# Performance work log

Measured on AMD Instinct MI355X. Metric: run time of the kernel, lower is better.

Reference implementation:

```python
import jax, jax.numpy as jnp
import numpy as np

N_NODES = 50000
N_EDGES = 625000
FEAT = 128
NEG_SLOPE = 0.2  # dgl GATConv default leaky_relu slope


def setup_inputs() -> dict:
    key = jax.random.key(0)
    ks = jax.random.split(key, 16)
    x = jax.random.normal(ks[0], (N_NODES, FEAT), dtype=jnp.float32)
    src = jax.random.randint(ks[1], (N_EDGES,), 0, N_NODES, dtype=jnp.int32)
    dst = jax.random.randint(ks[2], (N_EDGES,), 0, N_NODES, dtype=jnp.int32)
    s = 1.0 / np.sqrt(FEAT)
    d = {"x": x, "src": src, "dst": dst}
    for i in range(3):
        d[f"W{i+1}"] = jax.random.normal(ks[3 + 4 * i], (FEAT, FEAT), dtype=jnp.float32) * s
        d[f"al{i+1}"] = jax.random.normal(ks[4 + 4 * i], (FEAT,), dtype=jnp.float32) * s
        d[f"ar{i+1}"] = jax.random.normal(ks[5 + 4 * i], (FEAT,), dtype=jnp.float32) * s
        d[f"b{i+1}"] = jnp.zeros((FEAT,), dtype=jnp.float32)
    return d


def gat_layer(h_in, src, dst, W, al, ar, b):
    # dgl GATConv, num_heads=1: fc -> edge attention -> edge_softmax -> scatter
    h = h_in @ W                                   # [N, F]
    el = h @ al                                    # [N]
    er = h @ ar                                    # [N]
    e = jax.nn.leaky_relu(el[src] + er[dst], NEG_SLOPE)   # [E]
    # numerically stable edge softmax, grouped by destination node
    m = jax.ops.segment_max(e, dst, num_segments=N_NODES)  # [N]
    ex = jnp.exp(e - m[dst])
    denom = jax.ops.segment_sum(ex, dst, num_segments=N_NODES)
    alpha = ex / denom[dst]                        # [E]
    out = jax.ops.segment_sum(alpha[:, None] * h[src], dst, num_segments=N_NODES)
    return out + b


def reference(x, src, dst, W1, al1, ar1, b1, W2, al2, ar2, b2, W3, al3, ar3, b3):
    h = gat_layer(x, src, dst, W1, al1, ar1, b1)
    h = jax.nn.relu(h)
    h = gat_layer(h, src, dst, W2, al2, ar2, b2)
    h = jax.nn.relu(h)
    h = gat_layer(h, src, dst, W3, al3, ar3, b3)
    return h
```

## Files before the change

kernel.cpp:

```cpp
#include <hip/hip_runtime.h>
#include <hip/hip_fp16.h>

#define N_NODES 50000
#define N_EDGES 625000
#define FEAT 128
#define NEG_SLOPE 0.2f
#define NB_SCAN 196

typedef __attribute__((ext_vector_type(8))) short bf16x8;
typedef __attribute__((ext_vector_type(4))) float f32x4;

__device__ __forceinline__ unsigned short f2bf(float f) {
  unsigned u = __float_as_uint(f);
  u += 0x7fffu + ((u >> 16) & 1u);
  return (unsigned short)(u >> 16);
}
__device__ __forceinline__ float bf2f(unsigned short s) {
  return __uint_as_float(((unsigned)s) << 16);
}


__global__ __launch_bounds__(256) void prepzero_kernel(
    const float* __restrict__ W0, const float* __restrict__ W1, const float* __restrict__ W2,
    unsigned short* __restrict__ wfhi, unsigned short* __restrict__ wflo,
    int* __restrict__ cnt) {
  int bb = blockIdx.x;
  if (bb < 192) {
    int idx = bb * 256 + threadIdx.x;
    if (idx >= 3 * FEAT * FEAT) return;
    int l = idx >> 14, rem = idx & 16383;
    int e = rem & 7, lane = (rem >> 3) & 63, kb = (rem >> 9) & 3, ct = rem >> 11;
    int col = ct * 16 + (lane & 15);
    int k   = kb * 32 + (lane >> 4) * 8 + e;
    const float* W = (l == 0) ? W0 : ((l == 1) ? W1 : W2);
    float v = W[k * FEAT + col];
    unsigned short hi = f2bf(v);
    wfhi[idx] = hi;
    wflo[idx] = f2bf(v - bf2f(hi));
  } else {
    int i = (bb - 192) * 256 + threadIdx.x;
    if (i < N_NODES + 16) cnt[i] = 0;
  }
}


__global__ __launch_bounds__(256) void hist_kernel(const int* __restrict__ dst,
                                                   int* __restrict__ cnt) {
  int e = blockIdx.x * 256 + threadIdx.x;
  if (e < N_EDGES) atomicAdd(&cnt[dst[e]], 1);
}

__global__ __launch_bounds__(256) void scan_part_kernel(const int* __restrict__ cnt,
                                                        int* __restrict__ part) {
  __shared__ int s[256];
  int i = blockIdx.x * 256 + threadIdx.x;
  s[threadIdx.x] = (i < N_NODES) ? cnt[i] : 0;
  __syncthreads();
  for (int o = 128; o > 0; o >>= 1) {
    if (threadIdx.x < o) s[threadIdx.x] += s[threadIdx.x + o];
    __syncthreads();
  }
  if (threadIdx.x == 0) part[blockIdx.x] = s[0];
}

__global__ __launch_bounds__(256) void scan_down_kernel(int* __restrict__ cnt,
                                                        const int* __restrict__ part,
                                                        int* __restrict__ offs) {
  __shared__ int s[256];
  __shared__ int sl[256];
  const int tid = threadIdx.x;

  int pv = (tid < NB_SCAN) ? part[tid] : 0;
  s[tid] = pv;
  __syncthreads();
  for (int o = 1; o < 256; o <<= 1) {
    int t = (tid >= o) ? s[tid - o] : 0;
    __syncthreads();
    s[tid] += t;
    __syncthreads();
  }
  const int blockPrefix = (blockIdx.x == 0) ? 0 : s[blockIdx.x - 1];
  if (blockIdx.x == 0 && tid == 0) offs[N_NODES] = s[NB_SCAN - 1];

  int i = blockIdx.x * 256 + tid;
  int v = (i < N_NODES) ? cnt[i] : 0;
  sl[tid] = v;
  __syncthreads();
  for (int o = 1; o < 256; o <<= 1) {
    int t = (tid >= o) ? sl[tid - o] : 0;
    __syncthreads();
    sl[tid] += t;
    __syncthreads();
  }
  if (i < N_NODES) {
    int excl = sl[tid] - v + blockPrefix;
    offs[i] = excl;
    cnt[i] = excl;
  }
}

__global__ __launch_bounds__(256) void fill_kernel(const int* __restrict__ src,
                                                   const int* __restrict__ dst,
                                                   int* __restrict__ cursor,
                                                   int* __restrict__ ssrc) {
  int e = blockIdx.x * 256 + threadIdx.x;
  if (e < N_EDGES) {
    int pos = atomicAdd(&cursor[dst[e]], 1);
    ssrc[pos] = src[e];
  }
}


__global__ __launch_bounds__(256) void gemm_mfma_kernel(
    const float* __restrict__ inF, const __half* __restrict__ inH,
    const unsigned short* __restrict__ wfhi, const unsigned short* __restrict__ wflo,
    const float* __restrict__ al, const float* __restrict__ ar,
    __half* __restrict__ h, float* __restrict__ el, float* __restrict__ er,
    int fp16relu_in)
{
  __shared__ __align__(16) char smem[32768];
  unsigned short* wl = (unsigned short*)smem;
  typedef __half (*tile_t)[132];
  tile_t tile = (tile_t)smem;

  const int tid = threadIdx.x;
  const int wave = tid >> 6, lane = tid & 63;
  const int lrow = lane & 15, lkb = lane >> 4;
  const int arow_i = blockIdx.x * 64 + wave * 16 + lrow;
  const bool avalid = arow_i < N_NODES;

#pragma unroll
  for (int q = 0; q < 8; ++q) {
    int idx = q * 256 + tid;
    int hilo = idx >> 10, r = idx & 1023, frag = r >> 6, word = r & 63;
    int ct = frag >> 1, kb = frag & 1;
    const uint4* s4 = (const uint4*)(hilo ? wflo : wfhi);
    uint4 v = s4[(ct * 4 + kb) * 64 + word];
    *(uint4*)&wl[((hilo * 16 + frag) << 9) + word * 8] = v;
  }

  bf16x8 ahi[4], alo[4];
#pragma unroll
  for (int kb = 0; kb < 4; ++kb) {
    float a[8];
    if (avalid) {
      if (fp16relu_in) {
        const unsigned short* aH = (const unsigned short*)inH + (size_t)arow_i * FEAT;
        uint4 rv = *(const uint4*)(aH + kb * 32 + lkb * 8);
        const __half2* hp = (const __half2*)&rv;
#pragma unroll
        for (int e2 = 0; e2 < 4; ++e2) {
          float2 f = __half22float2(hp[e2]);
          a[e2 * 2] = fmaxf(f.x, 0.f); a[e2 * 2 + 1] = fmaxf(f.y, 0.f);
        }
      } else {
        const float* arow = inF + (size_t)arow_i * FEAT;
        float4 v0 = *(const float4*)(arow + kb * 32 + lkb * 8);
        float4 v1 = *(const float4*)(arow + kb * 32 + lkb * 8 + 4);
        a[0] = v0.x; a[1] = v0.y; a[2] = v0.z; a[3] = v0.w;
        a[4] = v1.x; a[5] = v1.y; a[6] = v1.z; a[7] = v1.w;
      }
    } else {
#pragma unroll
      for (int e = 0; e < 8; ++e) a[e] = 0.f;
    }
#pragma unroll
    for (int e = 0; e < 8; ++e) {
      unsigned short hb = f2bf(a[e]);
      ahi[kb][e] = (short)hb;
      alo[kb][e] = (short)f2bf(a[e] - bf2f(hb));
    }
  }

  f32x4 acc[8];
#pragma unroll
  for (int ct = 0; ct < 8; ++ct)
#pragma unroll
    for (int r = 0; r < 4; ++r) acc[ct][r] = 0.f;

  __syncthreads();
#pragma unroll
  for (int ct = 0; ct < 8; ++ct) {
#pragma unroll
    for (int kb1 = 0; kb1 < 2; ++kb1) {
      bf16x8 bhi = *(const bf16x8*)&wl[((ct * 2 + kb1) << 9) + lane * 8];
      bf16x8 blo = *(const bf16x8*)&wl[((16 + ct * 2 + kb1) << 9) + lane * 8];
      acc[ct] = __builtin_amdgcn_mfma_f32_16x16x32_bf16(ahi[kb1], bhi, acc[ct], 0, 0, 0);
      acc[ct] = __builtin_amdgcn_mfma_f32_16x16x32_bf16(ahi[kb1], blo, acc[ct], 0, 0, 0);
      acc[ct] = __builtin_amdgcn_mfma_f32_16x16x32_bf16(alo[kb1], bhi, acc[ct], 0, 0, 0);
    }
  }
  __syncthreads();

#pragma unroll
  for (int q = 0; q < 8; ++q) {
    int idx = q * 256 + tid;
    int hilo = idx >> 10, r = idx & 1023, frag = r >> 6, word = r & 63;
    int ct = frag >> 1, kb = 2 + (frag & 1);
    const uint4* s4 = (const uint4*)(hilo ? wflo : wfhi);
    uint4 v = s4[(ct * 4 + kb) * 64 + word];
    *(uint4*)&wl[((hilo * 16 + frag) << 9) + word * 8] = v;
  }
  __syncthreads();
#pragma unroll
  for (int ct = 0; ct < 8; ++ct) {
#pragma unroll
    for (int kb1 = 0; kb1 < 2; ++kb1) {
      bf16x8 bhi = *(const bf16x8*)&wl[((ct * 2 + kb1) << 9) + lane * 8];
      bf16x8 blo = *(const bf16x8*)&wl[((16 + ct * 2 + kb1) << 9) + lane * 8];
      acc[ct] = __builtin_amdgcn_mfma_f32_16x16x32_bf16(ahi[2 + kb1], bhi, acc[ct], 0, 0, 0);
      acc[ct] = __builtin_amdgcn_mfma_f32_16x16x32_bf16(ahi[2 + kb1], blo, acc[ct], 0, 0, 0);
      acc[ct] = __builtin_amdgcn_mfma_f32_16x16x32_bf16(alo[2 + kb1], bhi, acc[ct], 0, 0, 0);
    }
  }
  __syncthreads();

  float alv[8], arv[8];
#pragma unroll
  for (int ct = 0; ct < 8; ++ct) { alv[ct] = al[ct * 16 + lrow]; arv[ct] = ar[ct * 16 + lrow]; }

  const int lrow0 = wave * 16 + lkb * 4;
#pragma unroll
  for (int r = 0; r < 4; ++r) {
    float pel = 0.f, per_ = 0.f;
#pragma unroll
    for (int ct = 0; ct < 8; ++ct) {
      float v = acc[ct][r];
      tile[lrow0 + r][ct * 16 + lrow] = __float2half_rn(v);
      pel  = fmaf(v, alv[ct], pel);
      per_ = fmaf(v, arv[ct], per_);
    }
#pragma unroll
    for (int mask = 8; mask >= 1; mask >>= 1) {
      pel  += __shfl_xor(pel, mask);
      per_ += __shfl_xor(per_, mask);
    }
    int grow = blockIdx.x * 64 + lrow0 + r;
    if (grow < N_NODES && lrow == 0) { el[grow] = pel; er[grow] = per_; }
  }
  __syncthreads();

  const int row0g = blockIdx.x * 64;
#pragma unroll
  for (int it = 0; it < 4; ++it) {
    int idx = it * 256 + tid;
    int row = idx >> 4, c16 = idx & 15;
    int grow = row0g + row;
    if (grow < N_NODES) {
      uint4 v = *(const uint4*)&tile[row][c16 * 8];
      *((uint4*)(h + (size_t)grow * FEAT) + c16) = v;
    }
  }
}


__global__ __launch_bounds__(256) void agg_kernel(
    const __half* __restrict__ h, const float* __restrict__ el,
    const float* __restrict__ er, const int* __restrict__ offs,
    const int* __restrict__ ssrc, const float* __restrict__ bias,
    float* __restrict__ out32, __half* __restrict__ out16, int use16)
{
  const int tid = threadIdx.x;
  const int lane = tid & 63;
  const int qg = lane >> 4, ql = lane & 15;
  const int waveg = (blockIdx.x * 256 + tid) >> 6;
  const int node = waveg * 4 + qg;
  if (node >= N_NODES) return;

  const int beg = offs[node], end = offs[node + 1];
  const float erd = er[node];
  const unsigned short* __restrict__ hu = (const unsigned short*)h;
  const int qbase = qg * 16;

  float acc[8];
#pragma unroll
  for (int f = 0; f < 8; ++f) acc[f] = 0.f;
  float ds = 0.f;

  for (int base = beg; base < end; base += 16) {
    const int idx = base + ql;
    const bool v = idx < end;
    int s = 0;
    float ex = 0.f;
    if (v) s = ssrc[idx];
    if (v) {
      float t = el[s] + erd;
      t = t > 0.f ? t : NEG_SLOPE * t;
      ex = __expf(t);
    }
    ds += ex;

    const int ne = min(16, end - base);
    for (int j = 0; j < ne; j += 4) {
      int   s0 = __shfl(s,  qbase + j),     s1 = __shfl(s,  qbase + j + 1);
      int   s2 = __shfl(s,  qbase + j + 2), s3 = __shfl(s,  qbase + j + 3);
      float w0 = __shfl(ex, qbase + j),     w1 = __shfl(ex, qbase + j + 1);
      float w2 = __shfl(ex, qbase + j + 2), w3 = __shfl(ex, qbase + j + 3);
      uint4 r0 = *(const uint4*)(hu + (((size_t)s0) << 7) + (ql << 3));
      uint4 r1 = *(const uint4*)(hu + (((size_t)s1) << 7) + (ql << 3));
      uint4 r2 = *(const uint4*)(hu + (((size_t)s2) << 7) + (ql << 3));
      uint4 r3 = *(const uint4*)(hu + (((size_t)s3) << 7) + (ql << 3));
#pragma unroll
      for (int l = 0; l < 4; ++l) {
        const uint4& rr = (l == 0) ? r0 : (l == 1) ? r1 : (l == 2) ? r2 : r3;
        const float  ww = (l == 0) ? w0 : (l == 1) ? w1 : (l == 2) ? w2 : w3;
        float2 f0 = __half22float2(__builtin_bit_cast(__half2, rr.x));
        float2 f1 = __half22float2(__builtin_bit_cast(__half2, rr.y));
        float2 f2 = __half22float2(__builtin_bit_cast(__half2, rr.z));
        float2 f3 = __half22float2(__builtin_bit_cast(__half2, rr.w));
        acc[0] = fmaf(ww, f0.x, acc[0]); acc[1] = fmaf(ww, f0.y, acc[1]);
        acc[2] = fmaf(ww, f1.x, acc[2]); acc[3] = fmaf(ww, f1.y, acc[3]);
        acc[4] = fmaf(ww, f2.x, acc[4]); acc[5] = fmaf(ww, f2.y, acc[5]);
        acc[6] = fmaf(ww, f3.x, acc[6]); acc[7] = fmaf(ww, f3.y, acc[7]);
      }
    }
  }

#pragma unroll
  for (int mask = 8; mask >= 1; mask >>= 1) ds += __shfl_xor(ds, mask);
  const float inv = ds > 0.f ? 1.f / ds : 0.f;

  float4 b0 = ((const float4*)bias)[ql * 2];
  float4 b1 = ((const float4*)bias)[ql * 2 + 1];
  float o0 = fmaf(acc[0], inv, b0.x), o1 = fmaf(acc[1], inv, b0.y);
  float o2 = fmaf(acc[2], inv, b0.z), o3 = fmaf(acc[3], inv, b0.w);
  float o4 = fmaf(acc[4], inv, b1.x), o5 = fmaf(acc[5], inv, b1.y);
  float o6 = fmaf(acc[6], inv, b1.z), o7 = fmaf(acc[7], inv, b1.w);

  if (use16) {
    __half2 o[4];
    o[0] = __floats2half2_rn(o0, o1);
    o[1] = __floats2half2_rn(o2, o3);
    o[2] = __floats2half2_rn(o4, o5);
    o[3] = __floats2half2_rn(o6, o7);
    ((uint4*)(out16 + ((size_t)node << 7)))[ql] = *(const uint4*)o;
  } else {
    float4* op = (float4*)(out32 + ((size_t)node << 7)) + ql * 2;
    op[0] = make_float4(o0, o1, o2, o3);
    op[1] = make_float4(o4, o5, o6, o7);
  }
}


extern "C" void kernel_launch(void* const* d_in, const int* in_sizes, int n_in,
                              void* d_out, int out_size, void* d_ws, size_t ws_size,
                              hipStream_t stream) {
  const float* x  = (const float*)d_in[0];
  const int* src  = (const int*)d_in[1];
  const int* dst  = (const int*)d_in[2];
  const float* W[3]  = {(const float*)d_in[3],  (const float*)d_in[7],  (const float*)d_in[11]};
  const float* al[3] = {(const float*)d_in[4],  (const float*)d_in[8],  (const float*)d_in[12]};
  const float* ar[3] = {(const float*)d_in[5],  (const float*)d_in[9],  (const float*)d_in[13]};
  const float* b[3]  = {(const float*)d_in[6],  (const float*)d_in[10], (const float*)d_in[14]};

  __half* hH    = (__half*)d_ws;
  __half* out16 = hH + 6400000;
  float*  el    = (float*)(out16 + 6400000);
  float*  er    = el + 50016;
  int*    cnt   = (int*)(er + 50016);
  int*    offs  = cnt + 50016;
  int*    part  = offs + 50016;
  int*    ssrc  = part + 256;
  unsigned short* wfhi = (unsigned short*)(ssrc + 625000);
  unsigned short* wflo = wfhi + 3 * FEAT * FEAT;

  prepzero_kernel<<<392, 256, 0, stream>>>(W[0], W[1], W[2], wfhi, wflo, cnt);
  hist_kernel<<<(N_EDGES + 255) / 256, 256, 0, stream>>>(dst, cnt);
  scan_part_kernel<<<NB_SCAN, 256, 0, stream>>>(cnt, part);
  scan_down_kernel<<<NB_SCAN, 256, 0, stream>>>(cnt, part, offs);
  fill_kernel<<<(N_EDGES + 255) / 256, 256, 0, stream>>>(src, dst, cnt, ssrc);

  const int gemm_grid = (N_NODES + 63) / 64;
  const int agg_grid  = (N_NODES + 15) / 16;
  float* outf = (float*)d_out;

  for (int l = 0; l < 3; ++l) {
    gemm_mfma_kernel<<<gemm_grid, 256, 0, stream>>>(
        (l == 0) ? x : nullptr, (l == 0) ? nullptr : out16,
        wfhi + l * FEAT * FEAT, wflo + l * FEAT * FEAT,
        al[l], ar[l], hH, el, er, l > 0 ? 1 : 0);
    agg_kernel<<<agg_grid, 256, 0, stream>>>(
        hH, el, er, offs, ssrc, b[l], outf, out16, l < 2 ? 1 : 0);
  }
}
```

Measured before the change: 212.5 us.

## Fuse CSR build kernels into one cooperative kernel with grid syncs

Merges the weight-prep/zeroing, histogram, two scan passes and the fill pass into a single cooperative launch of 1024 blocks separated by grid-wide barriers. This removes four kernel launches and the gaps between them from the preprocessing chain. In exchange it adds grid.sync costs, uses grid-stride loops over edges with fewer blocks, and depends on all 1024 blocks being co-resident for the cooperative launch to succeed.

Measured after the change: 591.7 us. 178% more time.

```diff
diff --git a/kernel.cpp b/kernel.cpp
--- a/kernel.cpp
+++ b/kernel.cpp
@@ -1,11 +1,15 @@
 #include <hip/hip_runtime.h>
 #include <hip/hip_fp16.h>
+#include <hip/hip_cooperative_groups.h>
+
+namespace cg = cooperative_groups;
 
 #define N_NODES 50000
 #define N_EDGES 625000
 #define FEAT 128
 #define NEG_SLOPE 0.2f
 #define NB_SCAN 196
+#define CSR_GRID 1024
 
 typedef __attribute__((ext_vector_type(8))) short bf16x8;
 typedef __attribute__((ext_vector_type(4))) float f32x4;
@@ -20,92 +24,88 @@
 }
 
 
-__global__ __launch_bounds__(256) void prepzero_kernel(
+__global__ __launch_bounds__(256) void csr_fused_kernel(
     const float* __restrict__ W0, const float* __restrict__ W1, const float* __restrict__ W2,
     unsigned short* __restrict__ wfhi, unsigned short* __restrict__ wflo,
-    int* __restrict__ cnt) {
-  int bb = blockIdx.x;
-  if (bb < 192) {
-    int idx = bb * 256 + threadIdx.x;
-    if (idx >= 3 * FEAT * FEAT) return;
-    int l = idx >> 14, rem = idx & 16383;
-    int e = rem & 7, lane = (rem >> 3) & 63, kb = (rem >> 9) & 3, ct = rem >> 11;
-    int col = ct * 16 + (lane & 15);
-    int k   = kb * 32 + (lane >> 4) * 8 + e;
-    const float* W = (l == 0) ? W0 : ((l == 1) ? W1 : W2);
-    float v = W[k * FEAT + col];
-    unsigned short hi = f2bf(v);
-    wfhi[idx] = hi;
-    wflo[idx] = f2bf(v - bf2f(hi));
-  } else {
-    int i = (bb - 192) * 256 + threadIdx.x;
-    if (i < N_NODES + 16) cnt[i] = 0;
-  }
-}
-
-
-__global__ __launch_bounds__(256) void hist_kernel(const int* __restrict__ dst,
-                                                   int* __restrict__ cnt) {
-  int e = blockIdx.x * 256 + threadIdx.x;
-  if (e < N_EDGES) atomicAdd(&cnt[dst[e]], 1);
-}
-
-__global__ __launch_bounds__(256) void scan_part_kernel(const int* __restrict__ cnt,
-                                                        int* __restrict__ part) {
-  __shared__ int s[256];
-  int i = blockIdx.x * 256 + threadIdx.x;
-  s[threadIdx.x] = (i < N_NODES) ? cnt[i] : 0;
-  __syncthreads();
-  for (int o = 128; o > 0; o >>= 1) {
-    if (threadIdx.x < o) s[threadIdx.x] += s[threadIdx.x + o];
-    __syncthreads();
-  }
-  if (threadIdx.x == 0) part[blockIdx.x] = s[0];
-}
-
-__global__ __launch_bounds__(256) void scan_down_kernel(int* __restrict__ cnt,
-                                                        const int* __restrict__ part,
-                                                        int* __restrict__ offs) {
+    int* __restrict__ cnt, const int* __restrict__ dst, const int* __restrict__ src,
+    int* __restrict__ part, int* __restrict__ offs, int* __restrict__ ssrc)
+{
+  cg::grid_group grid = cg::this_grid();
+  const int tid = threadIdx.x;
   __shared__ int s[256];
   __shared__ int sl[256];
-  const int tid = threadIdx.x;
-
-  int pv = (tid < NB_SCAN) ? part[tid] : 0;
-  s[tid] = pv;
-  __syncthreads();
-  for (int o = 1; o < 256; o <<= 1) {
-    int t = (tid >= o) ? s[tid - o] : 0;
+
+  {
+    int bb = blockIdx.x;
+    if (bb < 192) {
+      int idx = bb * 256 + tid;
+      if (idx < 3 * FEAT * FEAT) {
+        int l = idx >> 14, rem = idx & 16383;
+        int e = rem & 7, lane = (rem >> 3) & 63, kb = (rem >> 9) & 3, ct = rem >> 11;
+        int col = ct * 16 + (lane & 15);
+        int k   = kb * 32 + (lane >> 4) * 8 + e;
+        const float* W = (l == 0) ? W0 : ((l == 1) ? W1 : W2);
+        float v = W[k * FEAT + col];
+        unsigned short hi = f2bf(v);
+        wfhi[idx] = hi;
+        wflo[idx] = f2bf(v - bf2f(hi));
+      }
+    } else if (bb < 392) {
+      int i = (bb - 192) * 256 + tid;
+      if (i < N_NODES + 16) cnt[i] = 0;
+    }
+  }
+  grid.sync();
+
+  for (int e = blockIdx.x * 256 + tid; e < N_EDGES; e += CSR_GRID * 256)
+    atomicAdd(&cnt[dst[e]], 1);
+  grid.sync();
+
+  if (blockIdx.x < NB_SCAN) {
+    int i = blockIdx.x * 256 + tid;
+    s[tid] = (i < N_NODES) ? cnt[i] : 0;
     __syncthreads();
-    s[tid] += t;
+    for (int o = 128; o > 0; o >>= 1) {
+      if (tid < o) s[tid] += s[tid + o];
+      __syncthreads();
+    }
+    if (tid == 0) part[blockIdx.x] = s[0];
+  }
+  grid.sync();
+
+  if (blockIdx.x < NB_SCAN) {
+    int pv = (tid < NB_SCAN) ? part[tid] : 0;
+    s[tid] = pv;
     __syncthreads();
-  }
-  const int blockPrefix = (blockIdx.x == 0) ? 0 : s[blockIdx.x - 1];
-  if (blockIdx.x == 0 && tid == 0) offs[N_NODES] = s[NB_SCAN - 1];
-
-  int i = blockIdx.x * 256 + tid;
-  int v = (i < N_NODES) ? cnt[i] : 0;
-  sl[tid] = v;
-  __syncthreads();
-  for (int o = 1; o < 256; o <<= 1) {
-    int t = (tid >= o) ? sl[tid - o] : 0;
+    for (int o = 1; o < 256; o <<= 1) {
+      int t = (tid >= o) ? s[tid - o] : 0;
+      __syncthreads();
+      s[tid] += t;
+      __syncthreads();
+    }
+    const int blockPrefix = (blockIdx.x == 0) ? 0 : s[blockIdx.x - 1];
+    if (blockIdx.x == 0 && tid == 0) offs[N_NODES] = s[NB_SCAN - 1];
+
+    int i = blockIdx.x * 256 + tid;
+    int v = (i < N_NODES) ? cnt[i] : 0;
+    sl[tid] = v;
     __syncthreads();
-    sl[tid] += t;
-    __syncthreads();
-  }
-  if (i < N_NODES) {
-    int excl = sl[tid] - v + blockPrefix;
-    offs[i] = excl;
-    cnt[i] = excl;
-  }
-}
-
-__global__ __launch_bounds__(256) void fill_kernel(const int* __restrict__ src,
-                                                   const int* __restrict__ dst,
-                                                   int* __restrict__ cursor,
-                                                   int* __restrict__ ssrc) {
-  int e = blockIdx.x * 256 + threadIdx.x;
-  if (e < N_EDGES) {
-    int pos = atomicAdd(&cursor[dst[e]], 1);
+    for (int o = 1; o < 256; o <<= 1) {
+      int t = (tid >= o) ? sl[tid - o] : 0;
+      __syncthreads();
+      sl[tid] += t;
+      __syncthreads();
+    }
+    if (i < N_NODES) {
+      int excl = sl[tid] - v + blockPrefix;
+      offs[i] = excl;
+      cnt[i] = excl;
+    }
+  }
+  grid.sync();
+
+  for (int e = blockIdx.x * 256 + tid; e < N_EDGES; e += CSR_GRID * 256) {
+    int pos = atomicAdd(&cnt[dst[e]], 1);
     ssrc[pos] = src[e];
   }
 }
@@ -364,11 +364,15 @@
   unsigned short* wfhi = (unsigned short*)(ssrc + 625000);
   unsigned short* wflo = wfhi + 3 * FEAT * FEAT;
 
-  prepzero_kernel<<<392, 256, 0, stream>>>(W[0], W[1], W[2], wfhi, wflo, cnt);
-  hist_kernel<<<(N_EDGES + 255) / 256, 256, 0, stream>>>(dst, cnt);
-  scan_part_kernel<<<NB_SCAN, 256, 0, stream>>>(cnt, part);
-  scan_down_kernel<<<NB_SCAN, 256, 0, stream>>>(cnt, part, offs);
-  fill_kernel<<<(N_EDGES + 255) / 256, 256, 0, stream>>>(src, dst, cnt, ssrc);
+  {
+    const float* W0 = W[0]; const float* W1 = W[1]; const float* W2 = W[2];
+    void* args[] = {(void*)&W0, (void*)&W1, (void*)&W2,
+                    (void*)&wfhi, (void*)&wflo, (void*)&cnt,
+                    (void*)&dst, (void*)&src, (void*)&part,
+                    (void*)&offs, (void*)&ssrc};
+    hipLaunchCooperativeKernel((void*)csr_fused_kernel, dim3(CSR_GRID), dim3(256),
+                               args, 0, stream);
+  }
 
   const int gemm_grid = (N_NODES + 63) / 64;
   const int agg_grid  = (N_NODES + 15) / 16;
```
